# Performance work log

Measured on AMD Instinct MI355X. Metric: run time of the kernel, lower is better.

## Reference

```python
import jax, jax.numpy as jnp
import numpy as np

B, N, E, D = 32, 4096, 8192, 128


def setup_inputs() -> dict:
    key = jax.random.key(0)
    ks = jax.random.split(key, 6)
    atom_state = jax.random.normal(ks[0], (B, N, D), dtype=jnp.float32)
    messages = jax.random.normal(ks[1], (B, E, D), dtype=jnp.float32)
    connectivity = jax.random.randint(ks[2], (B, E, 2), 0, N, dtype=jnp.int32)
    kernel = jax.random.normal(ks[3], (D, 3 * D), dtype=jnp.float32) * 0.05
    recurrent_kernel = jax.random.normal(ks[4], (D, 3 * D), dtype=jnp.float32) * 0.05
    bias = jnp.zeros((2, 3 * D), dtype=jnp.float32)
    return {"atom_state": atom_state, "messages": messages,
            "connectivity": connectivity, "kernel": kernel,
            "recurrent_kernel": recurrent_kernel, "bias": bias}


def reference(atom_state, messages, connectivity, kernel, recurrent_kernel, bias):
    b, n, d = atom_state.shape
    # --- Reduce: scatter-add messages onto target atoms ---
    tgt_idx = connectivity[:, :, 1]                       # [B,E]
    offset = (jnp.arange(b, dtype=tgt_idx.dtype) * n)[:, None]
    flat_idx = (tgt_idx + offset).reshape(-1)             # [B*E]
    flat_msgs = messages.reshape(-1, d)                   # [B*E,D]
    aggregated = jax.ops.segment_sum(flat_msgs, flat_idx, num_segments=b * n)  # [B*N,D]
    # --- GRUCell (Keras default: reset_after=True, sigmoid/tanh) ---
    h = atom_state.reshape(-1, d)                         # [B*N,D]
    matrix_x = aggregated @ kernel + bias[0]              # [B*N,3D]
    matrix_h = h @ recurrent_kernel + bias[1]             # [B*N,3D]
    x_z, x_r, x_h = jnp.split(matrix_x, 3, axis=-1)
    r_z, r_r, r_h = jnp.split(matrix_h, 3, axis=-1)
    z = jax.nn.sigmoid(x_z + r_z)
    r = jax.nn.sigmoid(x_r + r_r)
    hh = jnp.tanh(x_h + r * r_h)
    h_new = z * h + (1.0 - z) * hh
    return h_new.reshape(b, n, d)
```

## Files before the change

kernel.cpp:

```cpp
#include <hip/hip_runtime.h>
#include <hip/hip_bf16.h>
#include <stdint.h>

#define BB 32
#define NN 4096
#define EE 8192
#define DD 128
#define MM (BB * NN)
#define THREE_D (3 * DD)
#define CAP 32

typedef __bf16 bf16x8 __attribute__((ext_vector_type(8)));
typedef __bf16 bf16x2 __attribute__((ext_vector_type(2)));
typedef float  f32x4  __attribute__((ext_vector_type(4)));
typedef float  f32x2  __attribute__((ext_vector_type(2)));

#define AGG_BYTES ((size_t)MM * DD * 2)
#define WT_OFF    AGG_BYTES
#define WT_BYTES  ((size_t)2 * THREE_D * DD * 2)
#define CNT_OFF   (WT_OFF + WT_BYTES)
#define CNT_BYTES ((size_t)MM * 4)
#define BKT_OFF   (CNT_OFF + CNT_BYTES)

__global__ void transpose_weights(const float* __restrict__ w0,
                                  const float* __restrict__ w1,
                                  __bf16* __restrict__ wt,
                                  int* __restrict__ counts) {
    int tid = blockIdx.x * blockDim.x + threadIdx.x;
    for (int i = tid; i < MM; i += 2 * THREE_D * DD)
        counts[i] = 0;
    int mat = tid / (THREE_D * DD);
    int rem = tid % (THREE_D * DD);
    int col = rem / DD;
    int k   = rem % DD;
    const float* src = mat ? w1 : w0;
    wt[tid] = (__bf16)src[k * THREE_D + col];
}

__global__ void scatter_ids(const int* __restrict__ conn,
                            int* __restrict__ counts,
                            int* __restrict__ bucket) {
    int e = blockIdx.x * 256 + threadIdx.x;
    int b = e >> 13;
    int2 pr = ((const int2*)conn)[e];
    int node = b * NN + pr.y;
    int pos = atomicAdd(&counts[node], 1);
    if (pos < CAP) bucket[node * CAP + pos] = e;
}

__global__ void gather_messages(const float* __restrict__ messages,
                                const int* __restrict__ counts,
                                const int* __restrict__ bucket,
                                __bf16* __restrict__ agg) {
    int node = __builtin_amdgcn_readfirstlane(blockIdx.x * 16 + (threadIdx.x >> 6));
    int lane = threadIdx.x & 63;
    int cnt = counts[node];
    if (cnt > CAP) cnt = CAP;
    const int* bp = bucket + (size_t)node * CAP;
    float a0 = 0.f, a1 = 0.f;
    int i = 0;
    for (; i + 2 <= cnt; i += 2) {
        int e0 = bp[i];
        int e1 = bp[i + 1];
        f32x2 v0 = *(const f32x2*)(messages + (size_t)e0 * DD + lane * 2);
        f32x2 v1 = *(const f32x2*)(messages + (size_t)e1 * DD + lane * 2);
        a0 += v0[0] + v1[0];
        a1 += v0[1] + v1[1];
    }
    if (i < cnt) {
        int e = bp[i];
        f32x2 v = *(const f32x2*)(messages + (size_t)e * DD + lane * 2);
        a0 += v[0];
        a1 += v[1];
    }
    bf16x2 o;
    o[0] = (__bf16)a0;
    o[1] = (__bf16)a1;
    *(bf16x2*)(agg + (size_t)node * DD + lane * 2) = o;
}

#define TPB_GEMM 8
#define AGP 136
#define HP  132
__launch_bounds__(512, 2)
__global__ void gru_gemm_pipe(const __bf16* __restrict__ agg,
                              const float* __restrict__ h_in,
                              const __bf16* __restrict__ wt,
                              const float* __restrict__ bias,
                              float* __restrict__ out) {
    const int tid  = threadIdx.x;
    const int wave = tid >> 6;
    const int lane = tid & 63;
    const int quad = lane >> 4;
    const int l16  = lane & 15;

    __shared__ __bf16 aT[2][16 * AGP];
    __shared__ float  hT[2][16 * HP];

    bf16x8 bfrag[3][2][4];
    for (int p = 0; p < 3; ++p)
        for (int m = 0; m < 2; ++m)
            for (int ko = 0; ko < 4; ++ko)
                bfrag[p][m][ko] = *(const bf16x8*)(wt
                    + ((size_t)(m * THREE_D + p * 128 + wave * 16 + l16)) * DD
                    + ko * 32 + quad * 8);

    const int j = wave * 16 + l16;
    const float b0z = bias[j];
    const float b0r = bias[DD + j];
    const float b0h = bias[2 * DD + j];
    const float b1z = bias[THREE_D + j];
    const float b1r = bias[THREE_D + DD + j];
    const float b1h = bias[THREE_D + 2 * DD + j];

    const int tile0 = blockIdx.x * TPB_GEMM;

    bf16x8 sa;
    f32x4  sh;
    auto load_regs = [&](int tb) {
        if (tid < 256)
            sa = *(const bf16x8*)(agg + (size_t)tb * 2048 + tid * 8);
        sh = *(const f32x4*)(h_in + (size_t)tb * 2048 + tid * 4);
    };
    auto write_lds = [&](int buf) {
        if (tid < 256)
            *(bf16x8*)&aT[buf][(tid >> 4) * AGP + (tid & 15) * 8] = sa;
        *(f32x4*)&hT[buf][(tid >> 5) * HP + (tid & 31) * 4] = sh;
    };

    load_regs(tile0);
    write_lds(0);
    int buf = 0;
    for (int t = 0; t < TPB_GEMM; ++t) {
        __syncthreads();
        const int tb = tile0 + t;
        if (t + 1 < TPB_GEMM) load_regs(tb + 1);

        f32x4 acc[3][2];
        for (int p = 0; p < 3; ++p)
            for (int m = 0; m < 2; ++m)
                acc[p][m] = (f32x4){0.f, 0.f, 0.f, 0.f};

        for (int ko = 0; ko < 4; ++ko) {
            bf16x8 af = *(const bf16x8*)&aT[buf][l16 * AGP + ko * 32 + quad * 8];
            f32x4 h0 = *(const f32x4*)&hT[buf][l16 * HP + ko * 32 + quad * 8];
            f32x4 h1 = *(const f32x4*)&hT[buf][l16 * HP + ko * 32 + quad * 8 + 4];
            bf16x8 hg;
            for (int i = 0; i < 4; ++i) {
                hg[i]     = (__bf16)h0[i];
                hg[i + 4] = (__bf16)h1[i];
            }
            for (int p = 0; p < 3; ++p) {
                acc[p][0] = __builtin_amdgcn_mfma_f32_16x16x32_bf16(
                    af, bfrag[p][0][ko], acc[p][0], 0, 0, 0);
                acc[p][1] = __builtin_amdgcn_mfma_f32_16x16x32_bf16(
                    hg, bfrag[p][1][ko], acc[p][1], 0, 0, 0);
            }
        }

        for (int rr = 0; rr < 4; ++rr) {
            int rl  = quad * 4 + rr;
            int row = tb * 16 + rl;
            float xz  = acc[0][0][rr] + b0z;
            float rz  = acc[0][1][rr] + b1z;
            float xr  = acc[1][0][rr] + b0r;
            float rrg = acc[1][1][rr] + b1r;
            float xh  = acc[2][0][rr] + b0h;
            float rh  = acc[2][1][rr] + b1h;
            float z   = 1.f / (1.f + __expf(-(xz + rz)));
            float rg  = 1.f / (1.f + __expf(-(xr + rrg)));
            float pre = xh + rg * rh;
            float hh  = 2.f / (1.f + __expf(-2.f * pre)) - 1.f;
            float hold = hT[buf][rl * HP + j];
            float o = z * hold + (1.f - z) * hh;
            out[(size_t)row * DD + j] = o;
        }

        if (t + 1 < TPB_GEMM) write_lds(buf ^ 1);
        buf ^= 1;
    }
}

extern "C" void kernel_launch(void* const* d_in, const int* in_sizes, int n_in,
                              void* d_out, int out_size, void* d_ws, size_t ws_size,
                              hipStream_t stream) {
    const float* atom_state = (const float*)d_in[0];
    const float* messages   = (const float*)d_in[1];
    const int*   conn       = (const int*)d_in[2];
    const float* w0         = (const float*)d_in[3];
    const float* w1         = (const float*)d_in[4];
    const float* bias       = (const float*)d_in[5];
    float* out = (float*)d_out;

    __bf16* agg    = (__bf16*)d_ws;
    __bf16* wt     = (__bf16*)((char*)d_ws + WT_OFF);
    int*    counts = (int*)((char*)d_ws + CNT_OFF);
    int*    bucket = (int*)((char*)d_ws + BKT_OFF);

    transpose_weights<<<(2 * THREE_D * DD) / 256, 256, 0, stream>>>(w0, w1, wt, counts);
    scatter_ids<<<(BB * EE) / 256, 256, 0, stream>>>(conn, counts, bucket);
    gather_messages<<<MM / 16, 1024, 0, stream>>>(messages, counts, bucket, agg);
    gru_gemm_pipe<<<MM / (16 * TPB_GEMM), 512, 0, stream>>>(agg, atom_state, wt, bias, out);
}
```

Measured before the change: 362.4 us.

## Fuse message gather into GRU GEMM kernel with prefetched bucket reads

Removes the separate gather_messages kernel and its bf16 aggregate buffer. The GEMM kernel now gathers each 16-node tile's messages itself: it issues loads for the first four edges of the next tile before the MFMA loop and finishes the sum after it, then writes the bf16 result to LDS. This saves a full write and read of the aggregate array and one kernel launch. The cost is more registers, and only 256 of the 512 threads do the gather, which may limit memory-level parallelism compared with the dedicated kernel.

```diff
diff --git a/kernel.cpp b/kernel.cpp
--- a/kernel.cpp
+++ b/kernel.cpp
@@ -9,6 +9,7 @@
 #define MM (BB * NN)
 #define THREE_D (3 * DD)
 #define CAP 32
+#define PF 8
 
 typedef __bf16 bf16x8 __attribute__((ext_vector_type(8)));
 typedef __bf16 bf16x2 __attribute__((ext_vector_type(2)));
@@ -48,46 +49,17 @@
     if (pos < CAP) bucket[node * CAP + pos] = e;
 }
 
-__global__ void gather_messages(const float* __restrict__ messages,
-                                const int* __restrict__ counts,
-                                const int* __restrict__ bucket,
-                                __bf16* __restrict__ agg) {
-    int node = __builtin_amdgcn_readfirstlane(blockIdx.x * 16 + (threadIdx.x >> 6));
-    int lane = threadIdx.x & 63;
-    int cnt = counts[node];
-    if (cnt > CAP) cnt = CAP;
-    const int* bp = bucket + (size_t)node * CAP;
-    float a0 = 0.f, a1 = 0.f;
-    int i = 0;
-    for (; i + 2 <= cnt; i += 2) {
-        int e0 = bp[i];
-        int e1 = bp[i + 1];
-        f32x2 v0 = *(const f32x2*)(messages + (size_t)e0 * DD + lane * 2);
-        f32x2 v1 = *(const f32x2*)(messages + (size_t)e1 * DD + lane * 2);
-        a0 += v0[0] + v1[0];
-        a1 += v0[1] + v1[1];
-    }
-    if (i < cnt) {
-        int e = bp[i];
-        f32x2 v = *(const f32x2*)(messages + (size_t)e * DD + lane * 2);
-        a0 += v[0];
-        a1 += v[1];
-    }
-    bf16x2 o;
-    o[0] = (__bf16)a0;
-    o[1] = (__bf16)a1;
-    *(bf16x2*)(agg + (size_t)node * DD + lane * 2) = o;
-}
-
 #define TPB_GEMM 8
 #define AGP 136
 #define HP  132
 __launch_bounds__(512, 2)
-__global__ void gru_gemm_pipe(const __bf16* __restrict__ agg,
-                              const float* __restrict__ h_in,
-                              const __bf16* __restrict__ wt,
-                              const float* __restrict__ bias,
-                              float* __restrict__ out) {
+__global__ void gru_gemm_fused(const float* __restrict__ messages,
+                               const int* __restrict__ counts,
+                               const int* __restrict__ bucket,
+                               const float* __restrict__ h_in,
+                               const __bf16* __restrict__ wt,
+                               const float* __restrict__ bias,
+                               float* __restrict__ out) {
     const int tid  = threadIdx.x;
     const int wave = tid >> 6;
     const int lane = tid & 63;
@@ -115,26 +87,74 @@
 
     const int tile0 = blockIdx.x * TPB_GEMM;
 
-    bf16x8 sa;
-    f32x4  sh;
-    auto load_regs = [&](int tb) {
-        if (tid < 256)
-            sa = *(const bf16x8*)(agg + (size_t)tb * 2048 + tid * 8);
+    f32x4 sh;
+    auto load_h = [&](int tb) {
         sh = *(const f32x4*)(h_in + (size_t)tb * 2048 + tid * 4);
     };
-    auto write_lds = [&](int buf) {
-        if (tid < 256)
-            *(bf16x8*)&aT[buf][(tid >> 4) * AGP + (tid & 15) * 8] = sa;
-        *(f32x4*)&hT[buf][(tid >> 5) * HP + (tid & 31) * 4] = sh;
-    };
-
-    load_regs(tile0);
-    write_lds(0);
+    auto write_h = [&](int bf) {
+        *(f32x4*)&hT[bf][(tid >> 5) * HP + (tid & 31) * 4] = sh;
+    };
+
+    const int ar = tid >> 4;
+    const int ac = (tid & 15) * 8;
+    int cnt = 0;
+    int ids[PF];
+    f32x4 ma[4], mb[4];
+    auto agg_issue = [&](int tb) {
+        if (tid < 256) {
+            int node = tb * 16 + ar;
+            cnt = counts[node];
+            if (cnt > CAP) cnt = CAP;
+            *(int4*)&ids[0] = *(const int4*)(bucket + (size_t)node * CAP);
+            *(int4*)&ids[4] = *(const int4*)(bucket + (size_t)node * CAP + 4);
+            for (int i = 0; i < 4; ++i) {
+                int e = (i < cnt) ? ids[i] : 0;
+                ma[i] = *(const f32x4*)(messages + (size_t)e * DD + ac);
+                mb[i] = *(const f32x4*)(messages + (size_t)e * DD + ac + 4);
+            }
+        }
+    };
+    auto agg_finish = [&](int tb, int bf) {
+        if (tid < 256) {
+            f32x4 s0 = (f32x4){0.f, 0.f, 0.f, 0.f};
+            f32x4 s1 = (f32x4){0.f, 0.f, 0.f, 0.f};
+            for (int i = 0; i < 4; ++i)
+                if (i < cnt) { s0 += ma[i]; s1 += mb[i]; }
+            if (cnt > 4) {
+                for (int i = 4; i < 8; ++i) {
+                    int e = (i < cnt) ? ids[i] : 0;
+                    f32x4 va = *(const f32x4*)(messages + (size_t)e * DD + ac);
+                    f32x4 vb = *(const f32x4*)(messages + (size_t)e * DD + ac + 4);
+                    if (i < cnt) { s0 += va; s1 += vb; }
+                }
+                for (int i = PF; i < cnt; ++i) {
+                    int e = bucket[(size_t)(tb * 16 + ar) * CAP + i];
+                    s0 += *(const f32x4*)(messages + (size_t)e * DD + ac);
+                    s1 += *(const f32x4*)(messages + (size_t)e * DD + ac + 4);
+                }
+            }
+            bf16x8 o;
+            for (int q = 0; q < 4; ++q) {
+                o[q]     = (__bf16)s0[q];
+                o[q + 4] = (__bf16)s1[q];
+            }
+            *(bf16x8*)&aT[bf][ar * AGP + ac] = o;
+        }
+    };
+
+    agg_issue(tile0);
+    load_h(tile0);
+    agg_finish(tile0, 0);
+    write_h(0);
+
     int buf = 0;
     for (int t = 0; t < TPB_GEMM; ++t) {
         __syncthreads();
         const int tb = tile0 + t;
-        if (t + 1 < TPB_GEMM) load_regs(tb + 1);
+        if (t + 1 < TPB_GEMM) {
+            agg_issue(tb + 1);
+            load_h(tb + 1);
+        }
 
         f32x4 acc[3][2];
         for (int p = 0; p < 3; ++p)
@@ -157,6 +177,8 @@
                     hg, bfrag[p][1][ko], acc[p][1], 0, 0, 0);
             }
         }
+
+        if (t + 1 < TPB_GEMM) agg_finish(tb + 1, buf ^ 1);
 
         for (int rr = 0; rr < 4; ++rr) {
             int rl  = quad * 4 + rr;
@@ -176,7 +198,7 @@
             out[(size_t)row * DD + j] = o;
         }
 
-        if (t + 1 < TPB_GEMM) write_lds(buf ^ 1);
+        if (t + 1 < TPB_GEMM) write_h(buf ^ 1);
         buf ^= 1;
     }
 }
@@ -192,13 +214,12 @@
     const float* bias       = (const float*)d_in[5];
     float* out = (float*)d_out;
 
-    __bf16* agg    = (__bf16*)d_ws;
     __bf16* wt     = (__bf16*)((char*)d_ws + WT_OFF);
     int*    counts = (int*)((char*)d_ws + CNT_OFF);
     int*    bucket = (int*)((char*)d_ws + BKT_OFF);
 
     transpose_weights<<<(2 * THREE_D * DD) / 256, 256, 0, stream>>>(w0, w1, wt, counts);
     scatter_ids<<<(BB * EE) / 256, 256, 0, stream>>>(conn, counts, bucket);
-    gather_messages<<<MM / 16, 1024, 0, stream>>>(messages, counts, bucket, agg);
-    gru_gemm_pipe<<<MM / (16 * TPB_GEMM), 512, 0, stream>>>(agg, atom_state, wt, bias, out);
-}
+    gru_gemm_fused<<<MM / (16 * TPB_GEMM), 512, 0, stream>>>(
+        messages, counts, bucket, atom_state, wt, bias, out);
+}
```

New measurement: 345.9 us. -4.5%, faster.
